# Kernel optimization log

Measured on AMD Instinct MI355X. Metric: run time of the kernel, lower is better.

Reference implementation:

```python
import jax, jax.numpy as jnp
import numpy as np

TEMPERATURE = 8.0      # sqrt(d_head=64), matches init temperature
MASK_FILL = -1e32      # masked_softmax memory_efficient fill value
B, L, D = 16, 2048, 64


def setup_inputs() -> dict:
    key = jax.random.key(0)
    kq, kk, kv, kd, km = jax.random.split(key, 5)
    q = jax.random.normal(kq, (B, L, D), dtype=jnp.float32)
    k = jax.random.normal(kk, (B, L, D), dtype=jnp.float32)
    v = jax.random.normal(kv, (B, L, D), dtype=jnp.float32)
    diag_mask = jax.random.randint(kd, (B, L, L), 0, 2, dtype=jnp.int32)  # 1=keep, 0=mask
    mask = jax.random.randint(km, (B, L, L), 0, 2, dtype=jnp.int32).astype(jnp.bool_)  # True=mask out
    return {"q": q, "k": k, "v": v, "diag_mask": diag_mask, "mask": mask}


def reference(q, k, v, diag_mask, mask):
    # attn = q @ k^T / temperature   -> [B, Lq, Lk]
    attn = jnp.einsum('bqd,bkd->bqk', q, k) / TEMPERATURE
    # attn.masked_fill(mask, -inf)
    attn = jnp.where(mask, -jnp.inf, attn)
    # masked_softmax(attn, diag_mask, memory_efficient=True):
    #   masked_fill((1 - diag_mask).bool(), -1e32) then softmax
    attn = jnp.where(diag_mask == 0, MASK_FILL, attn)
    attn = jax.nn.softmax(attn, axis=-1)
    # output = attn @ v
    output = jnp.einsum('bqk,bkd->bqd', attn, v)
    return output, attn
```

## Files before the change

kernel.cpp:

```cpp
#include <hip/hip_runtime.h>
#include <math.h>

#define NB 16
#define SL 2048
#define HD 64
#define TQ 16
#define BK 64
#define NT (SL / BK)
#define SC2 0.18033688f
#define SSTRIDE 2056

typedef _Float16 half8 __attribute__((ext_vector_type(8)));
typedef float floatx4 __attribute__((ext_vector_type(4)));
typedef int intx4 __attribute__((ext_vector_type(4)));

__device__ __forceinline__ half8 load_frag_f32(const float* p) {
  floatx4 f0 = *(const floatx4*)p;
  floatx4 f1 = *(const floatx4*)(p + 4);
  half8 h;
  h[0] = (_Float16)f0[0]; h[1] = (_Float16)f0[1];
  h[2] = (_Float16)f0[2]; h[3] = (_Float16)f0[3];
  h[4] = (_Float16)f1[0]; h[5] = (_Float16)f1[1];
  h[6] = (_Float16)f1[2]; h[7] = (_Float16)f1[3];
  return h;
}

__global__ __launch_bounds__(256) void prep_pack_kernel(
    const float* __restrict__ K, const float* __restrict__ V,
    const int* __restrict__ DM, const int* __restrict__ MMk,
    _Float16* __restrict__ KH, _Float16* __restrict__ VT,
    unsigned char* __restrict__ BITS)
{
  const int bid = blockIdx.x;
  const int t   = (int)threadIdx.x;

  if (bid < 2048) {
    const size_t r0 = (size_t)bid * 16;
    #pragma unroll 4
    for (int r = 0; r < 16; ++r) {
      const size_t off = (r0 + r) * SL + (size_t)t * 8;
      intx4 d0 = __builtin_nontemporal_load((const intx4*)(DM + off));
      intx4 d1 = __builtin_nontemporal_load((const intx4*)(DM + off + 4));
      intx4 m0 = __builtin_nontemporal_load((const intx4*)(MMk + off));
      intx4 m1 = __builtin_nontemporal_load((const intx4*)(MMk + off + 4));
      unsigned byte = 0;
      #pragma unroll
      for (int j = 0; j < 4; ++j) {
        byte |= (unsigned)((d0[j] & ~m0[j]) & 1) << j;
        byte |= (unsigned)((d1[j] & ~m1[j]) & 1) << (j + 4);
      }
      BITS[(r0 + r) * (SL / 8) + t] = (unsigned char)byte;
    }
    return;
  }

  __shared__ __align__(16) _Float16 tile[64][72];
  const int pb = bid - 2048;
  const int k0 = (pb & 31) * 64;
  const int b  = pb >> 5;
  const size_t base = (size_t)b * SL * HD;
  const int r  = t >> 2;
  const int cq = (t & 3) * 16;

  const float* kp = K + base + (size_t)(k0 + r) * HD + cq;
  const float* vp = V + base + (size_t)(k0 + r) * HD + cq;
  half8 kh0 = load_frag_f32(kp), kh1 = load_frag_f32(kp + 8);
  half8 vh0 = load_frag_f32(vp), vh1 = load_frag_f32(vp + 8);

  _Float16* khp = KH + base + (size_t)(k0 + r) * HD + cq;
  *(half8*)khp       = kh0;
  *(half8*)(khp + 8) = kh1;

  const int wc = cq ^ (((r >> 4) & 3) * 16);
  *(half8*)&tile[r][wc]     = vh0;
  *(half8*)&tile[r][wc + 8] = vh1;
  __syncthreads();

  const int sx = ((cq >> 4) & 3) * 16;
  half8 o0, o1;
  #pragma unroll
  for (int i = 0; i < 8; ++i) {
    o0[i] = tile[cq + i][r ^ sx];
    o1[i] = tile[cq + 8 + i][r ^ sx];
  }
  _Float16* vt = VT + (size_t)b * HD * SL + (size_t)r * SL + k0 + cq;
  *(half8*)vt       = o0;
  *(half8*)(vt + 8) = o1;
}

template <int MODE>
__global__ __launch_bounds__(512, 4) void attn_kernel(
    const float* __restrict__ Q, const float* __restrict__ K,
    const float* __restrict__ V, const _Float16* __restrict__ KH,
    const _Float16* __restrict__ VT, const unsigned char* __restrict__ BITS,
    const int* __restrict__ DM, const int* __restrict__ MMk,
    float* __restrict__ Out, float* __restrict__ Attn)
{
  const int qt    = blockIdx.x;
  const int b     = blockIdx.y;
  const int tid   = (int)threadIdx.x;
  const int w     = tid >> 6;
  const int w4    = w & 3;
  const int hf    = w >> 2;
  const int lane  = tid & 63;
  const int quad  = lane >> 4;
  const int nl    = lane & 15;
  const int row16 = tid >> 5;
  const int ci    = tid & 31;

  const int qbase    = qt * TQ;
  const size_t bLD   = (size_t)b * SL * HD;
  const size_t mbase = ((size_t)b * SL + qbase) * SL;

  __shared__ __align__(16) _Float16 S[TQ * SSTRIDE];
  __shared__ float sinv_s[TQ];
  __shared__ float obuf[TQ][65];

  unsigned Wlo = 0, Whi = 0;
  if constexpr (MODE == 2) {
    const unsigned long long* browp =
        (const unsigned long long*)BITS + ((size_t)b * SL + qbase) * (SL / 64);
    const unsigned long long Wll = browp[tid];
    Wlo = (unsigned)Wll;
    Whi = (unsigned)(Wll >> 32);
  }

  half8 aq0, aq1;
  {
    const float* qp = Q + bLD + (size_t)(qbase + nl) * HD + quad * 8;
    aq0 = load_frag_f32(qp);
    aq1 = load_frag_f32(qp + 32);
  }

  const int kt0 = hf * (NT / 2);
  #pragma unroll 2
  for (int kti = 0; kti < NT / 2; ++kti) {
    const int kt = kt0 + kti;
    half8 bk0, bk1;
    if constexpr (MODE >= 1) {
      const _Float16* kp = KH + bLD + (size_t)(kt * BK + w4 * 16 + nl) * HD + quad * 8;
      bk0 = *(const half8*)kp;
      bk1 = *(const half8*)(kp + 32);
    } else {
      const float* kp = K + bLD + (size_t)(kt * BK + w4 * 16 + nl) * HD + quad * 8;
      bk0 = load_frag_f32(kp);
      bk1 = load_frag_f32(kp + 32);
    }
    floatx4 acc = {0.f, 0.f, 0.f, 0.f};
    acc = __builtin_amdgcn_mfma_f32_16x16x32_f16(aq0, bk0, acc, 0, 0, 0);
    acc = __builtin_amdgcn_mfma_f32_16x16x32_f16(aq1, bk1, acc, 0, 0, 0);
    const int col = kt * BK + w4 * 16 + nl;
    #pragma unroll
    for (int r = 0; r < 4; ++r)
      S[(quad * 4 + r) * SSTRIDE + col] = (_Float16)(acc[r] * SC2);
  }
  __syncthreads();

  _Float16* srow = &S[row16 * SSTRIDE];
  float sum = 0.f;
  if constexpr (MODE == 2) {
    const bool useLo = (ci & 4) == 0;
    const int  bsh   = (ci & 3) * 8;
    #pragma unroll
    for (int it = 0; it < 8; ++it) {
      const int c    = it * 256 + ci * 8;
      const int srcl = (lane & 32) | (it * 4 + (ci >> 3));
      const unsigned lo = __shfl(Wlo, srcl, 64);
      const unsigned hi = __shfl(Whi, srcl, 64);
      const unsigned kb = ((useLo ? lo : hi) >> bsh) & 0xFFu;
      half8 s8 = *(const half8*)(srow + c);
      half8 e8;
      #pragma unroll
      for (int j = 0; j < 4; ++j) {
        const float e0 = (kb & (1u << j))       ? __builtin_amdgcn_exp2f((float)s8[j])     : 0.f;
        const float e1 = (kb & (1u << (j + 4))) ? __builtin_amdgcn_exp2f((float)s8[j + 4]) : 0.f;
        sum += e0 + e1;
        e8[j]     = (_Float16)e0;
        e8[j + 4] = (_Float16)e1;
      }
      *(half8*)(srow + c) = e8;
    }
  } else {
    const int* dmr = DM  + mbase + (size_t)row16 * SL;
    const int* mkr = MMk + mbase + (size_t)row16 * SL;
    #pragma unroll 4
    for (int it = 0; it < 8; ++it) {
      const int c = it * 256 + ci * 8;
      intx4 d0 = __builtin_nontemporal_load((const intx4*)(dmr + c));
      intx4 d1 = __builtin_nontemporal_load((const intx4*)(dmr + c + 4));
      intx4 m0 = __builtin_nontemporal_load((const intx4*)(mkr + c));
      intx4 m1 = __builtin_nontemporal_load((const intx4*)(mkr + c + 4));
      half8 s8 = *(const half8*)(srow + c);
      half8 e8;
      #pragma unroll
      for (int j = 0; j < 4; ++j) {
        const int keep0 = d0[j] & ~m0[j];
        const int keep1 = d1[j] & ~m1[j];
        const float e0 = keep0 ? __builtin_amdgcn_exp2f((float)s8[j])     : 0.f;
        const float e1 = keep1 ? __builtin_amdgcn_exp2f((float)s8[j + 4]) : 0.f;
        sum += e0 + e1;
        e8[j]     = (_Float16)e0;
        e8[j + 4] = (_Float16)e1;
      }
      *(half8*)(srow + c) = e8;
    }
  }
  #pragma unroll
  for (int off = 1; off < 32; off <<= 1)
    sum += __shfl_xor(sum, off, 64);
  const float is = (sum > 0.f) ? 1.f / sum : 0.f;
  if (ci == 0) sinv_s[row16] = is;
  __syncthreads();

  const float isr = sinv_s[row16];
  float* arow = Attn + mbase + (size_t)row16 * SL;
  floatx4 oacc = {0.f, 0.f, 0.f, 0.f};
  #pragma unroll
  for (int kti = 0; kti < NT / 2; ++kti) {
    const int kt = kt0 + kti;
    half8 ap0 = *(const half8*)(&S[nl * SSTRIDE + kt * BK + quad * 8]);
    half8 ap1 = *(const half8*)(&S[nl * SSTRIDE + kt * BK + quad * 8 + 32]);
    half8 bv0, bv1;
    if constexpr (MODE >= 1) {
      const _Float16* vp = VT + bLD + (size_t)(w4 * 16 + nl) * SL + kt * BK + quad * 8;
      bv0 = *(const half8*)vp;
      bv1 = *(const half8*)(vp + 32);
    } else {
      const float* vp = V + bLD + (size_t)(kt * BK + quad * 8) * HD + w4 * 16 + nl;
      #pragma unroll
      for (int j = 0; j < 8; ++j) {
        bv0[j] = (_Float16)vp[(size_t)j * HD];
        bv1[j] = (_Float16)vp[(size_t)(j + 32) * HD];
      }
    }
    oacc = __builtin_amdgcn_mfma_f32_16x16x32_f16(ap0, bv0, oacc, 0, 0, 0);
    oacc = __builtin_amdgcn_mfma_f32_16x16x32_f16(ap1, bv1, oacc, 0, 0, 0);
    if ((kti & 1) == 0) {
      const int c = (kti >> 1) * 256 + ci * 8;
      half8 e8v = *(const half8*)(srow + c);
      floatx4 o0, o1;
      #pragma unroll
      for (int j = 0; j < 4; ++j) {
        o0[j] = (float)e8v[j]     * isr;
        o1[j] = (float)e8v[j + 4] * isr;
      }
      __builtin_nontemporal_store(o0, (floatx4*)(arow + c));
      __builtin_nontemporal_store(o1, (floatx4*)(arow + c + 4));
    }
  }

  if (hf == 1) {
    #pragma unroll
    for (int r = 0; r < 4; ++r)
      obuf[quad * 4 + r][w4 * 16 + nl] = oacc[r];
  }
  __syncthreads();
  if (hf == 0) {
    float* op = Out + ((size_t)b * SL + qbase) * HD;
    #pragma unroll
    for (int r = 0; r < 4; ++r) {
      const int row = quad * 4 + r;
      op[(size_t)row * HD + w4 * 16 + nl] =
          (oacc[r] + obuf[row][w4 * 16 + nl]) * sinv_s[row];
    }
  }
}

extern "C" void kernel_launch(void* const* d_in, const int* in_sizes, int n_in,
                              void* d_out, int out_size, void* d_ws, size_t ws_size,
                              hipStream_t stream) {
  const float* Q  = (const float*)d_in[0];
  const float* K  = (const float*)d_in[1];
  const float* V  = (const float*)d_in[2];
  const int* DM   = (const int*)d_in[3];
  const int* MMk  = (const int*)d_in[4];
  float* Out  = (float*)d_out;
  float* Attn = (float*)d_out + (size_t)NB * SL * HD;
  dim3 grid(SL / TQ, NB);

  const size_t needKV   = (size_t)2 * NB * SL * HD * sizeof(_Float16);
  const size_t needBits = (size_t)NB * SL * (SL / 8);
  if (d_ws != nullptr && ws_size >= needKV + needBits) {
    _Float16* KH = (_Float16*)d_ws;
    _Float16* VT = KH + (size_t)NB * SL * HD;
    unsigned char* BITS = (unsigned char*)(VT + (size_t)NB * SL * HD);
    prep_pack_kernel<<<dim3(2048 + 512), 256, 0, stream>>>(K, V, DM, MMk, KH, VT, BITS);
    attn_kernel<2><<<grid, 512, 0, stream>>>(Q, K, V, KH, VT, BITS, DM, MMk, Out, Attn);
  } else if (d_ws != nullptr && ws_size >= needKV) {
    _Float16* KH = (_Float16*)d_ws;
    _Float16* VT = KH + (size_t)NB * SL * HD;
    prep_pack_kernel<<<dim3(512), 256, 0, stream>>>(K, V, DM, MMk, KH, VT, nullptr);
    attn_kernel<1><<<grid, 512, 0, stream>>>(Q, K, V, KH, VT, nullptr, DM, MMk, Out, Attn);
  } else {
    attn_kernel<0><<<grid, 512, 0, stream>>>(Q, K, V, nullptr, nullptr, nullptr, DM, MMk, Out, Attn);
  }
}
```

Before: 696.3 us.

## Fuse mask and exp into the QK^T epilogue with per-wave partial row sums

The masked exp2 and row-sum computation moves into the QK^T MFMA epilogue. Mask bits are staged in shared memory and each lane reads them directly, so the separate pass that re-read S and shuffled the bit words is gone. Row sums are reduced within each wave by shuffles and combined across waves through a small shared array, which adds one extra barrier. The prep kernel block order is also swapped so the K/V pack blocks run first (512 on the K/V path), which lets the attention kernel depend on them sooner.

Measured after the change: 717.3 us. 3.0% more time.

```diff
diff --git a/kernel.cpp b/kernel.cpp
--- a/kernel.cpp
+++ b/kernel.cpp
@@ -34,8 +34,8 @@
   const int bid = blockIdx.x;
   const int t   = (int)threadIdx.x;
 
-  if (bid < 2048) {
-    const size_t r0 = (size_t)bid * 16;
+  if (bid >= 512) {
+    const size_t r0 = (size_t)(bid - 512) * 16;
     #pragma unroll 4
     for (int r = 0; r < 16; ++r) {
       const size_t off = (r0 + r) * SL + (size_t)t * 8;
@@ -55,9 +55,8 @@
   }
 
   __shared__ __align__(16) _Float16 tile[64][72];
-  const int pb = bid - 2048;
-  const int k0 = (pb & 31) * 64;
-  const int b  = pb >> 5;
+  const int k0 = (bid & 31) * 64;
+  const int b  = bid >> 5;
   const size_t base = (size_t)b * SL * HD;
   const int r  = t >> 2;
   const int cq = (t & 3) * 16;
@@ -113,16 +112,16 @@
   const size_t mbase = ((size_t)b * SL + qbase) * SL;
 
   __shared__ __align__(16) _Float16 S[TQ * SSTRIDE];
+  __shared__ __align__(8) unsigned char bitsRM[TQ][264];
   __shared__ float sinv_s[TQ];
+  __shared__ float partial[TQ][9];
   __shared__ float obuf[TQ][65];
 
-  unsigned Wlo = 0, Whi = 0;
   if constexpr (MODE == 2) {
     const unsigned long long* browp =
         (const unsigned long long*)BITS + ((size_t)b * SL + qbase) * (SL / 64);
-    const unsigned long long Wll = browp[tid];
-    Wlo = (unsigned)Wll;
-    Whi = (unsigned)(Wll >> 32);
+    const unsigned long long wbits = browp[tid];
+    *(unsigned long long*)&bitsRM[tid >> 5][(tid & 31) * 8] = wbits;
   }
 
   half8 aq0, aq1;
@@ -131,8 +130,10 @@
     aq0 = load_frag_f32(qp);
     aq1 = load_frag_f32(qp + 32);
   }
+  if constexpr (MODE == 2) __syncthreads();
 
   const int kt0 = hf * (NT / 2);
+  float rsum[4] = {0.f, 0.f, 0.f, 0.f};
   #pragma unroll 2
   for (int kti = 0; kti < NT / 2; ++kti) {
     const int kt = kt0 + kti;
@@ -150,39 +151,51 @@
     acc = __builtin_amdgcn_mfma_f32_16x16x32_f16(aq0, bk0, acc, 0, 0, 0);
     acc = __builtin_amdgcn_mfma_f32_16x16x32_f16(aq1, bk1, acc, 0, 0, 0);
     const int col = kt * BK + w4 * 16 + nl;
+    if constexpr (MODE == 2) {
+      const unsigned char* bp = &bitsRM[0][0] + (quad * 4) * 264 + kt * 8 + w4 * 2;
+      #pragma unroll
+      for (int r = 0; r < 4; ++r) {
+        const unsigned short mb = *(const unsigned short*)(bp + r * 264);
+        const float e = ((mb >> nl) & 1)
+                            ? __builtin_amdgcn_exp2f(acc[r] * SC2) : 0.f;
+        S[(quad * 4 + r) * SSTRIDE + col] = (_Float16)e;
+        rsum[r] += e;
+      }
+    } else {
+      #pragma unroll
+      for (int r = 0; r < 4; ++r)
+        S[(quad * 4 + r) * SSTRIDE + col] = (_Float16)(acc[r] * SC2);
+    }
+  }
+
+  if constexpr (MODE == 2) {
     #pragma unroll
-    for (int r = 0; r < 4; ++r)
-      S[(quad * 4 + r) * SSTRIDE + col] = (_Float16)(acc[r] * SC2);
-  }
-  __syncthreads();
-
-  _Float16* srow = &S[row16 * SSTRIDE];
-  float sum = 0.f;
-  if constexpr (MODE == 2) {
-    const bool useLo = (ci & 4) == 0;
-    const int  bsh   = (ci & 3) * 8;
-    #pragma unroll
-    for (int it = 0; it < 8; ++it) {
-      const int c    = it * 256 + ci * 8;
-      const int srcl = (lane & 32) | (it * 4 + (ci >> 3));
-      const unsigned lo = __shfl(Wlo, srcl, 64);
-      const unsigned hi = __shfl(Whi, srcl, 64);
-      const unsigned kb = ((useLo ? lo : hi) >> bsh) & 0xFFu;
-      half8 s8 = *(const half8*)(srow + c);
-      half8 e8;
-      #pragma unroll
-      for (int j = 0; j < 4; ++j) {
-        const float e0 = (kb & (1u << j))       ? __builtin_amdgcn_exp2f((float)s8[j])     : 0.f;
-        const float e1 = (kb & (1u << (j + 4))) ? __builtin_amdgcn_exp2f((float)s8[j + 4]) : 0.f;
-        sum += e0 + e1;
-        e8[j]     = (_Float16)e0;
-        e8[j + 4] = (_Float16)e1;
-      }
-      *(half8*)(srow + c) = e8;
-    }
+    for (int r = 0; r < 4; ++r) {
+      float v = rsum[r];
+      v += __shfl_xor(v, 1, 64);
+      v += __shfl_xor(v, 2, 64);
+      v += __shfl_xor(v, 4, 64);
+      v += __shfl_xor(v, 8, 64);
+      rsum[r] = v;
+    }
+    if (nl == 0) {
+      #pragma unroll
+      for (int r = 0; r < 4; ++r) partial[quad * 4 + r][w] = rsum[r];
+    }
+    __syncthreads();
+    if (tid < 16) {
+      float s = 0.f;
+      #pragma unroll
+      for (int wi = 0; wi < 8; ++wi) s += partial[tid][wi];
+      sinv_s[tid] = (s > 0.f) ? 1.f / s : 0.f;
+    }
+    __syncthreads();
   } else {
+    __syncthreads();
+    _Float16* srow0 = &S[row16 * SSTRIDE];
     const int* dmr = DM  + mbase + (size_t)row16 * SL;
     const int* mkr = MMk + mbase + (size_t)row16 * SL;
+    float sum = 0.f;
     #pragma unroll 4
     for (int it = 0; it < 8; ++it) {
       const int c = it * 256 + ci * 8;
@@ -190,7 +203,7 @@
       intx4 d1 = __builtin_nontemporal_load((const intx4*)(dmr + c + 4));
       intx4 m0 = __builtin_nontemporal_load((const intx4*)(mkr + c));
       intx4 m1 = __builtin_nontemporal_load((const intx4*)(mkr + c + 4));
-      half8 s8 = *(const half8*)(srow + c);
+      half8 s8 = *(const half8*)(srow0 + c);
       half8 e8;
       #pragma unroll
       for (int j = 0; j < 4; ++j) {
@@ -202,17 +215,18 @@
         e8[j]     = (_Float16)e0;
         e8[j + 4] = (_Float16)e1;
       }
-      *(half8*)(srow + c) = e8;
-    }
-  }
-  #pragma unroll
-  for (int off = 1; off < 32; off <<= 1)
-    sum += __shfl_xor(sum, off, 64);
-  const float is = (sum > 0.f) ? 1.f / sum : 0.f;
-  if (ci == 0) sinv_s[row16] = is;
-  __syncthreads();
+      *(half8*)(srow0 + c) = e8;
+    }
+    #pragma unroll
+    for (int off = 1; off < 32; off <<= 1)
+      sum += __shfl_xor(sum, off, 64);
+    const float is = (sum > 0.f) ? 1.f / sum : 0.f;
+    if (ci == 0) sinv_s[row16] = is;
+    __syncthreads();
+  }
 
   const float isr = sinv_s[row16];
+  _Float16* srow = &S[row16 * SSTRIDE];
   float* arow = Attn + mbase + (size_t)row16 * SL;
   floatx4 oacc = {0.f, 0.f, 0.f, 0.f};
   #pragma unroll
@@ -284,7 +298,7 @@
     _Float16* KH = (_Float16*)d_ws;
     _Float16* VT = KH + (size_t)NB * SL * HD;
     unsigned char* BITS = (unsigned char*)(VT + (size_t)NB * SL * HD);
-    prep_pack_kernel<<<dim3(2048 + 512), 256, 0, stream>>>(K, V, DM, MMk, KH, VT, BITS);
+    prep_pack_kernel<<<dim3(512 + 2048), 256, 0, stream>>>(K, V, DM, MMk, KH, VT, BITS);
     attn_kernel<2><<<grid, 512, 0, stream>>>(Q, K, V, KH, VT, BITS, DM, MMk, Out, Attn);
   } else if (d_ws != nullptr && ws_size >= needKV) {
     _Float16* KH = (_Float16*)d_ws;
```

## Halve query tile to 8 rows, one wave per softmax row, reorder prep blocks

Applied to the files above, without the earlier changes.

Cuts the attention block's query tile from 16 to 8 rows, which halves the LDS score buffer and raises the occupancy hint from 4 to 8 blocks per CU. The MFMA tiles stay 16 wide, so half of each MFMA's rows are duplicates whose results are thrown away. Each wave now owns one softmax row and reads its mask bits from a shared-memory copy instead of using lane shuffles. The prep kernel also runs its K/V pack blocks before the mask-bit blocks. The cost is doubled K/V fragment loads per query row and wasted MFMA work, in exchange for more blocks resident at once.

After: 853.1 us. 1.23x slower.

```diff
diff --git a/kernel.cpp b/kernel.cpp
--- a/kernel.cpp
+++ b/kernel.cpp
@@ -4,7 +4,7 @@
 #define NB 16
 #define SL 2048
 #define HD 64
-#define TQ 16
+#define TQ 8
 #define BK 64
 #define NT (SL / BK)
 #define SC2 0.18033688f
@@ -34,8 +34,8 @@
   const int bid = blockIdx.x;
   const int t   = (int)threadIdx.x;
 
-  if (bid < 2048) {
-    const size_t r0 = (size_t)bid * 16;
+  if (bid >= 512) {
+    const size_t r0 = (size_t)(bid - 512) * 16;
     #pragma unroll 4
     for (int r = 0; r < 16; ++r) {
       const size_t off = (r0 + r) * SL + (size_t)t * 8;
@@ -55,9 +55,8 @@
   }
 
   __shared__ __align__(16) _Float16 tile[64][72];
-  const int pb = bid - 2048;
-  const int k0 = (pb & 31) * 64;
-  const int b  = pb >> 5;
+  const int k0 = (bid & 31) * 64;
+  const int b  = bid >> 5;
   const size_t base = (size_t)b * SL * HD;
   const int r  = t >> 2;
   const int cq = (t & 3) * 16;
@@ -89,7 +88,7 @@
 }
 
 template <int MODE>
-__global__ __launch_bounds__(512, 4) void attn_kernel(
+__global__ __launch_bounds__(512, 8) void attn_kernel(
     const float* __restrict__ Q, const float* __restrict__ K,
     const float* __restrict__ V, const _Float16* __restrict__ KH,
     const _Float16* __restrict__ VT, const unsigned char* __restrict__ BITS,
@@ -105,29 +104,25 @@
   const int lane  = tid & 63;
   const int quad  = lane >> 4;
   const int nl    = lane & 15;
-  const int row16 = tid >> 5;
-  const int ci    = tid & 31;
 
   const int qbase    = qt * TQ;
   const size_t bLD   = (size_t)b * SL * HD;
   const size_t mbase = ((size_t)b * SL + qbase) * SL;
 
   __shared__ __align__(16) _Float16 S[TQ * SSTRIDE];
+  __shared__ unsigned bitsW[512];
   __shared__ float sinv_s[TQ];
   __shared__ float obuf[TQ][65];
 
-  unsigned Wlo = 0, Whi = 0;
   if constexpr (MODE == 2) {
-    const unsigned long long* browp =
-        (const unsigned long long*)BITS + ((size_t)b * SL + qbase) * (SL / 64);
-    const unsigned long long Wll = browp[tid];
-    Wlo = (unsigned)Wll;
-    Whi = (unsigned)(Wll >> 32);
+    const unsigned* bp =
+        (const unsigned*)(BITS + ((size_t)b * SL + qbase) * (SL / 8));
+    bitsW[tid] = bp[tid];
   }
 
   half8 aq0, aq1;
   {
-    const float* qp = Q + bLD + (size_t)(qbase + nl) * HD + quad * 8;
+    const float* qp = Q + bLD + (size_t)(qbase + (nl & 7)) * HD + quad * 8;
     aq0 = load_frag_f32(qp);
     aq1 = load_frag_f32(qp + 32);
   }
@@ -150,24 +145,22 @@
     acc = __builtin_amdgcn_mfma_f32_16x16x32_f16(aq0, bk0, acc, 0, 0, 0);
     acc = __builtin_amdgcn_mfma_f32_16x16x32_f16(aq1, bk1, acc, 0, 0, 0);
     const int col = kt * BK + w4 * 16 + nl;
-    #pragma unroll
-    for (int r = 0; r < 4; ++r)
-      S[(quad * 4 + r) * SSTRIDE + col] = (_Float16)(acc[r] * SC2);
-  }
-  __syncthreads();
-
-  _Float16* srow = &S[row16 * SSTRIDE];
+    if (quad < 2) {
+      #pragma unroll
+      for (int r = 0; r < 4; ++r)
+        S[(quad * 4 + r) * SSTRIDE + col] = (_Float16)(acc[r] * SC2);
+    }
+  }
+  __syncthreads();
+
+  _Float16* srow = &S[w * SSTRIDE];
   float sum = 0.f;
   if constexpr (MODE == 2) {
-    const bool useLo = (ci & 4) == 0;
-    const int  bsh   = (ci & 3) * 8;
-    #pragma unroll
-    for (int it = 0; it < 8; ++it) {
-      const int c    = it * 256 + ci * 8;
-      const int srcl = (lane & 32) | (it * 4 + (ci >> 3));
-      const unsigned lo = __shfl(Wlo, srcl, 64);
-      const unsigned hi = __shfl(Whi, srcl, 64);
-      const unsigned kb = ((useLo ? lo : hi) >> bsh) & 0xFFu;
+    const unsigned char* bl = (const unsigned char*)bitsW;
+    #pragma unroll
+    for (int it = 0; it < 4; ++it) {
+      const int c = it * 512 + lane * 8;
+      const unsigned kb = bl[w * 256 + it * 64 + lane];
       half8 s8 = *(const half8*)(srow + c);
       half8 e8;
       #pragma unroll
@@ -181,11 +174,11 @@
       *(half8*)(srow + c) = e8;
     }
   } else {
-    const int* dmr = DM  + mbase + (size_t)row16 * SL;
-    const int* mkr = MMk + mbase + (size_t)row16 * SL;
-    #pragma unroll 4
-    for (int it = 0; it < 8; ++it) {
-      const int c = it * 256 + ci * 8;
+    const int* dmr = DM  + mbase + (size_t)w * SL;
+    const int* mkr = MMk + mbase + (size_t)w * SL;
+    #pragma unroll
+    for (int it = 0; it < 4; ++it) {
+      const int c = it * 512 + lane * 8;
       intx4 d0 = __builtin_nontemporal_load((const intx4*)(dmr + c));
       intx4 d1 = __builtin_nontemporal_load((const intx4*)(dmr + c + 4));
       intx4 m0 = __builtin_nontemporal_load((const intx4*)(mkr + c));
@@ -206,20 +199,19 @@
     }
   }
   #pragma unroll
-  for (int off = 1; off < 32; off <<= 1)
+  for (int off = 1; off < 64; off <<= 1)
     sum += __shfl_xor(sum, off, 64);
-  const float is = (sum > 0.f) ? 1.f / sum : 0.f;
-  if (ci == 0) sinv_s[row16] = is;
-  __syncthreads();
-
-  const float isr = sinv_s[row16];
-  float* arow = Attn + mbase + (size_t)row16 * SL;
+  if (lane == 0) sinv_s[w] = (sum > 0.f) ? 1.f / sum : 0.f;
+  __syncthreads();
+
+  const float isr = sinv_s[w];
+  float* arow = Attn + mbase + (size_t)w * SL;
   floatx4 oacc = {0.f, 0.f, 0.f, 0.f};
   #pragma unroll
   for (int kti = 0; kti < NT / 2; ++kti) {
     const int kt = kt0 + kti;
-    half8 ap0 = *(const half8*)(&S[nl * SSTRIDE + kt * BK + quad * 8]);
-    half8 ap1 = *(const half8*)(&S[nl * SSTRIDE + kt * BK + quad * 8 + 32]);
+    half8 ap0 = *(const half8*)(&S[(nl & 7) * SSTRIDE + kt * BK + quad * 8]);
+    half8 ap1 = *(const half8*)(&S[(nl & 7) * SSTRIDE + kt * BK + quad * 8 + 32]);
     half8 bv0, bv1;
     if constexpr (MODE >= 1) {
       const _Float16* vp = VT + bLD + (size_t)(w4 * 16 + nl) * SL + kt * BK + quad * 8;
@@ -235,8 +227,8 @@
     }
     oacc = __builtin_amdgcn_mfma_f32_16x16x32_f16(ap0, bv0, oacc, 0, 0, 0);
     oacc = __builtin_amdgcn_mfma_f32_16x16x32_f16(ap1, bv1, oacc, 0, 0, 0);
-    if ((kti & 1) == 0) {
-      const int c = (kti >> 1) * 256 + ci * 8;
+    if ((kti & 3) == 0) {
+      const int c = (kti >> 2) * 512 + lane * 8;
       half8 e8v = *(const half8*)(srow + c);
       floatx4 o0, o1;
       #pragma unroll
@@ -249,13 +241,13 @@
     }
   }
 
-  if (hf == 1) {
+  if (hf == 1 && quad < 2) {
     #pragma unroll
     for (int r = 0; r < 4; ++r)
       obuf[quad * 4 + r][w4 * 16 + nl] = oacc[r];
   }
   __syncthreads();
-  if (hf == 0) {
+  if (hf == 0 && quad < 2) {
     float* op = Out + ((size_t)b * SL + qbase) * HD;
     #pragma unroll
     for (int r = 0; r < 4; ++r) {
@@ -284,7 +276,7 @@
     _Float16* KH = (_Float16*)d_ws;
     _Float16* VT = KH + (size_t)NB * SL * HD;
     unsigned char* BITS = (unsigned char*)(VT + (size_t)NB * SL * HD);
-    prep_pack_kernel<<<dim3(2048 + 512), 256, 0, stream>>>(K, V, DM, MMk, KH, VT, BITS);
+    prep_pack_kernel<<<dim3(512 + 2048), 256, 0, stream>>>(K, V, DM, MMk, KH, VT, BITS);
     attn_kernel<2><<<grid, 512, 0, stream>>>(Q, K, V, KH, VT, BITS, DM, MMk, Out, Attn);
   } else if (d_ws != nullptr && ws_size >= needKV) {
     _Float16* KH = (_Float16*)d_ws;
```
